# Kernel tuning notes

Measured on AMD Instinct MI355X. Metric: run time of the kernel, lower is better.

Reference implementation:

```python
import jax, jax.numpy as jnp
import numpy as np

B, T, C, H = 2, 2048, 1024, 16


def setup_inputs() -> dict:
    key = jax.random.key(0)
    ks = jax.random.split(key, 9)
    s = 1.0 / np.sqrt(C)
    return {
        "query": jax.random.normal(ks[0], (B, T, C), dtype=jnp.float32),
        "Wq": jax.random.normal(ks[1], (C, C), dtype=jnp.float32) * s,
        "bq": jnp.zeros((C,), dtype=jnp.float32),
        "Wk": jax.random.normal(ks[2], (C, C), dtype=jnp.float32) * s,
        "bk": jnp.zeros((C,), dtype=jnp.float32),
        "Wv": jax.random.normal(ks[3], (C, C), dtype=jnp.float32) * s,
        "bv": jnp.zeros((C,), dtype=jnp.float32),
        "Wp": jax.random.normal(ks[4], (C, C), dtype=jnp.float32) * s,
        "bp": jnp.zeros((C,), dtype=jnp.float32),
        "n_head": H,
    }


def reference(query, Wq, bq, Wk, bk, Wv, bv, Wp, bp, n_head):
    b, t, c = query.shape
    d = c // n_head
    # QKV projections -> [b, h, t, d]
    q = (query @ Wq + bq).reshape(b, t, n_head, d).transpose(0, 2, 1, 3)
    k = (query @ Wk + bk).reshape(b, t, n_head, d).transpose(0, 2, 1, 3)
    v = (query @ Wv + bv).reshape(b, t, n_head, d).transpose(0, 2, 1, 3)
    scale = 1.0 / jnp.sqrt(jnp.asarray(d, dtype=query.dtype))
    att = jnp.einsum('bhtd,bhsd->bhts', q, k) * scale  # [b,h,t,t]
    causal = jnp.tril(jnp.ones((t, t), dtype=bool))
    att = jnp.where(causal[None, None, :, :], att, -jnp.inf)
    att = jax.nn.softmax(att, axis=-1)
    y = jnp.einsum('bhts,bhsd->bhtd', att, v)  # [b,h,t,d]
    y = y.transpose(0, 2, 1, 3).reshape(b, t, c)
    return y @ Wp + bp
```

## Files before the change

### kernel.cpp

```cpp
#include <hip/hip_runtime.h>
#include <math.h>

#define B_ 2
#define T_ 2048
#define C_ 1024
#define H_ 16
#define D_ 64
#define M_ (B_*T_)

typedef __bf16 bf16x8 __attribute__((ext_vector_type(8)));
typedef __bf16 bf16x4 __attribute__((ext_vector_type(4)));
typedef float  f32x4  __attribute__((ext_vector_type(4)));

__device__ __forceinline__ unsigned short f2bf(float f) {
    unsigned int u = __float_as_uint(f);
    u += 0x7FFFu + ((u >> 16) & 1u);
    return (unsigned short)(u >> 16);
}

__device__ __forceinline__ void gload16(const void* g, void* l) {
    __builtin_amdgcn_global_load_lds(
        (const __attribute__((address_space(1))) void*)g,
        (__attribute__((address_space(3))) void*)l, 16, 0, 0);
}

__global__ __launch_bounds__(256) void prep_kernel(
    const float* __restrict__ X, unsigned short* __restrict__ Xb,
    const float* __restrict__ W0, const float* __restrict__ W1,
    const float* __restrict__ W2, const float* __restrict__ W3,
    unsigned short* __restrict__ T0, unsigned short* __restrict__ T1,
    unsigned short* __restrict__ T2, unsigned short* __restrict__ T3)
{
    const int tid = threadIdx.x;
    if (blockIdx.x < 2048) {
        const size_t i = ((size_t)blockIdx.x * 256 + tid) * 8;
        const float4 a = *(const float4*)&X[i];
        const float4 b = *(const float4*)&X[i + 4];
        ushort4 s0, s1;
        s0.x = f2bf(a.x); s0.y = f2bf(a.y); s0.z = f2bf(a.z); s0.w = f2bf(a.w);
        s1.x = f2bf(b.x); s1.y = f2bf(b.y); s1.z = f2bf(b.z); s1.w = f2bf(b.w);
        *(ushort4*)&Xb[i]     = s0;
        *(ushort4*)&Xb[i + 4] = s1;
        return;
    }
    const int bz = blockIdx.x - 2048;
    const int z = bz >> 10, rem = bz & 1023;
    const float* W; unsigned short* Wt;
    switch (z) {
        case 0: W = W0; Wt = T0; break;
        case 1: W = W1; Wt = T1; break;
        case 2: W = W2; Wt = T2; break;
        default: W = W3; Wt = T3; break;
    }
    __shared__ unsigned short tile[32][33];
    const int k0 = (rem >> 5) * 32, n0 = (rem & 31) * 32;
    {
        const int r = tid >> 3, c = (tid & 7) * 4;
        const float4 v = *(const float4*)&W[(size_t)(k0 + r)*C_ + n0 + c];
        tile[c+0][r] = f2bf(v.x);
        tile[c+1][r] = f2bf(v.y);
        tile[c+2][r] = f2bf(v.z);
        tile[c+3][r] = f2bf(v.w);
    }
    __syncthreads();
    {
        const int r = tid >> 3, c = (tid & 7) * 4;
        ushort4 s;
        s.x = tile[r][c+0]; s.y = tile[r][c+1]; s.z = tile[r][c+2]; s.w = tile[r][c+3];
        *(ushort4*)&Wt[(size_t)(n0 + r)*C_ + k0 + c] = s;
    }
}

__global__ __launch_bounds__(256) void gemm_mfma_kernel(
    const unsigned short* __restrict__ A, const unsigned short* __restrict__ Bt,
    const float* __restrict__ b0, const float* __restrict__ b1,
    const float* __restrict__ b2,
    void* __restrict__ out0, void* __restrict__ out1, void* __restrict__ out2,
    int mode)
{
    __shared__ __align__(16) unsigned short Als[2][128 * 32];
    __shared__ __align__(16) unsigned short Bls[2][128 * 32];

    const int tid  = threadIdx.x;
    const int lane = tid & 63;
    const int wave = tid >> 6;
    const int wm = wave >> 1, wn = wave & 1;
    const int l15 = lane & 15, quad = lane >> 4;
    const int m0 = blockIdx.y * 128, n0 = blockIdx.x * 128;
    const int srow = lane >> 2;
    const int scol = (lane & 3) * 8;

    const f32x4 zero4 = {0.f, 0.f, 0.f, 0.f};
    f32x4 acc[4][4];
    #pragma unroll
    for (int i = 0; i < 4; ++i)
        #pragma unroll
        for (int j = 0; j < 4; ++j) acc[i][j] = zero4;

    for (int k0 = 0; k0 < C_; k0 += 64) {
        __syncthreads();
        #pragma unroll
        for (int h = 0; h < 2; ++h) {
            #pragma unroll
            for (int u = 0; u < 2; ++u) {
                const int r = wave*32 + u*16 + srow;
                gload16(&A [(size_t)(m0 + r)*C_ + k0 + h*32 + scol],
                        &Als[h][(wave*32 + u*16)*32]);
                gload16(&Bt[(size_t)(n0 + r)*C_ + k0 + h*32 + scol],
                        &Bls[h][(wave*32 + u*16)*32]);
            }
        }
        __syncthreads();

        #pragma unroll
        for (int h = 0; h < 2; ++h) {
            bf16x8 af[4], bfr[4];
            #pragma unroll
            for (int i = 0; i < 4; ++i)
                af[i] = *(const bf16x8*)&Als[h][(wm*64 + i*16 + l15)*32 + quad*8];
            #pragma unroll
            for (int j = 0; j < 4; ++j)
                bfr[j] = *(const bf16x8*)&Bls[h][(wn*64 + j*16 + l15)*32 + quad*8];

            #pragma unroll
            for (int i = 0; i < 4; ++i)
                #pragma unroll
                for (int j = 0; j < 4; ++j)
                    acc[i][j] = __builtin_amdgcn_mfma_f32_16x16x32_bf16(
                        af[i], bfr[j], acc[i][j], 0, 0, 0);
        }
    }

    if (mode == 0) {
        float* o0 = (float*)out0;
        #pragma unroll
        for (int j = 0; j < 4; ++j) {
            const int n = n0 + wn*64 + j*16 + l15;
            const float bias = b0[n];
            #pragma unroll
            for (int i = 0; i < 4; ++i)
                #pragma unroll
                for (int r = 0; r < 4; ++r) {
                    const int m = m0 + wm*64 + i*16 + quad*4 + r;
                    o0[(size_t)m*C_ + n] = acc[i][j][r] + bias;
                }
        }
        return;
    }

    __syncthreads();
    unsigned short* Ep = (wave < 2) ? &Als[wave][0] : &Bls[wave - 2][0];

    const int which = n0 >> 10;
    const int c0 = n0 & (C_ - 1);
    const int h  = (c0 >> 6) + wn;
    const int bb = m0 >> 11;
    const int t0 = (m0 & (T_ - 1)) + wm*64;
    const int bh = bb*H_ + h;
    const float* bp = (which == 0) ? b0 : (which == 1 ? b1 : b2);
    const float qscale = (which == 0) ? 0.125f : 1.0f;

    if (which < 2) {
        #pragma unroll
        for (int j = 0; j < 4; ++j) {
            const int cl = j*16 + l15;
            const float bias = bp[c0 + wn*64 + cl];
            #pragma unroll
            for (int i = 0; i < 4; ++i)
                #pragma unroll
                for (int r = 0; r < 4; ++r)
                    Ep[(i*16 + quad*4 + r)*64 + cl] =
                        f2bf((acc[i][j][r] + bias) * qscale);
        }
        unsigned short* op = (which == 0) ? (unsigned short*)out0
                                          : (unsigned short*)out1;
        const int chunk = lane & 7;
        #pragma unroll
        for (int u = 0; u < 8; ++u) {
            const int row = u*8 + (lane >> 3);
            const uint4 v = *(const uint4*)&Ep[row*64 + chunk*8];
            *(uint4*)&op[((size_t)bh*T_ + t0 + row)*D_ + chunk*8] = v;
        }
    } else {
        #pragma unroll
        for (int j = 0; j < 4; ++j) {
            const int cl = j*16 + l15;
            const float bias = bp[c0 + wn*64 + cl];
            const int xo = (l15 & 7) * 8;
            #pragma unroll
            for (int i = 0; i < 4; ++i) {
                ushort4 pk;
                pk.x = f2bf(acc[i][j][0] + bias);
                pk.y = f2bf(acc[i][j][1] + bias);
                pk.z = f2bf(acc[i][j][2] + bias);
                pk.w = f2bf(acc[i][j][3] + bias);
                *(ushort4*)&Ep[cl*64 + ((i*16 + quad*4) ^ xo)] = pk;
            }
        }
        unsigned short* op = (unsigned short*)out2;
        const int chunk = lane & 7;
        #pragma unroll
        for (int u = 0; u < 8; ++u) {
            const int d = u*8 + (lane >> 3);
            const uint4 v = *(const uint4*)&Ep[d*64 + ((chunk*8) ^ ((d & 7)*8))];
            *(uint4*)&op[((size_t)bh*D_ + d)*T_ + t0 + chunk*8] = v;
        }
    }
}

__global__ __launch_bounds__(256) void flash_mfma_kernel(
    const unsigned short* __restrict__ Qs, const unsigned short* __restrict__ Ks,
    const unsigned short* __restrict__ Vts, unsigned short* __restrict__ Y,
    float* __restrict__ parts, float* __restrict__ lbase)
{
    __shared__ __align__(16) unsigned short Kls[64 * 64];
    __shared__ __align__(16) unsigned short Vls[64 * 64];
    __shared__ __align__(16) unsigned short Pls[4 * 2048];

    const int tid  = threadIdx.x;
    const int lane = tid & 63, wave = tid >> 6;
    const int l15  = lane & 15, quad = lane >> 4;
    const int job  = blockIdx.x >> 5;
    const int bh   = blockIdx.x & 31;
    const bool isA = (job < 8);
    const int a    = isA ? job : job - 8;

    int qts[2], slos[2], shis[2], slots[2], nseg;
    if (isA) {
        qts[0] = a;      slos[0] = 0;        shis[0] = 2*a + 2;  slots[0] = -1;
        qts[1] = 15 - a; slos[1] = 0;        shis[1] = 15 - 2*a; slots[1] = 0;
        nseg = 2;
    } else {
        qts[0] = 15 - a; slos[0] = 15 - 2*a; shis[0] = 32 - 2*a; slots[0] = 1;
        nseg = 1;
    }

    unsigned short* Pw = &Pls[wave * 2048];
    const int kd_s = wave >> 1;
    const int c8_s = (kd_s * 4 + quad) * 8;
    const int b_ = bh >> 4, h_ = bh & (H_ - 1);
    const f32x4 zero4 = {0.f, 0.f, 0.f, 0.f};

    for (int sg = 0; sg < nseg; ++sg) {
        const int qt  = qts[sg];
        const int qw0 = qt * 128 + wave * 32;

        bf16x8 qf[2][2];
        #pragma unroll
        for (int i = 0; i < 2; ++i)
            #pragma unroll
            for (int kd = 0; kd < 2; ++kd)
                qf[i][kd] = *(const bf16x8*)&Qs[((size_t)bh*T_ + qw0 + i*16 + l15)*D_
                                                + kd*32 + quad*8];

        f32x4 o[2][4];
        #pragma unroll
        for (int i = 0; i < 2; ++i)
            #pragma unroll
            for (int jd = 0; jd < 4; ++jd) o[i][jd] = zero4;
        float lsum[2] = {0.f, 0.f};

        for (int it = slos[sg]; it < shis[sg]; ++it) {
            const int s0 = it * 64;
            __syncthreads();
            #pragma unroll
            for (int u = 0; u < 2; ++u) {
                const int cu  = 2*wave + u;
                const int row = ((cu & 3) << 4) + l15;
                gload16(&Ks [((size_t)bh*T_ + s0 + row)*D_ + c8_s],
                        (char*)Kls + cu*1024);
                gload16(&Vts[((size_t)bh*D_ + row)*T_ + s0 + c8_s],
                        (char*)Vls + cu*1024);
            }
            __syncthreads();

            if (s0 > qw0 + 31) continue;

            f32x4 st[2][4];
            #pragma unroll
            for (int i = 0; i < 2; ++i)
                #pragma unroll
                for (int j = 0; j < 4; ++j) st[i][j] = zero4;
            #pragma unroll
            for (int kd = 0; kd < 2; ++kd) {
                bf16x8 kf[4];
                #pragma unroll
                for (int j = 0; j < 4; ++j)
                    kf[j] = *(const bf16x8*)&Kls[lane*8 + j*512 + kd*2048];
                #pragma unroll
                for (int i = 0; i < 2; ++i)
                    #pragma unroll
                    for (int j = 0; j < 4; ++j)
                        st[i][j] = __builtin_amdgcn_mfma_f32_16x16x32_bf16(
                            kf[j], qf[i][kd], st[i][j], 0, 0, 0);
            }

            const bool diag = (s0 + 63 > qw0);
            #pragma unroll
            for (int i = 0; i < 2; ++i) {
                const int qrow = qw0 + i*16 + l15;
                #pragma unroll
                for (int j = 0; j < 4; ++j)
                    #pragma unroll
                    for (int r = 0; r < 4; ++r) {
                        float e = __expf(st[i][j][r]);
                        if (diag && (s0 + j*16 + quad*4 + r > qrow)) e = 0.f;
                        st[i][j][r] = e;
                        lsum[i] += e;
                    }
            }

            #pragma unroll
            for (int i = 0; i < 2; ++i)
                #pragma unroll
                for (int j = 0; j < 4; ++j) {
                    bf16x4 pk = {(__bf16)st[i][j][0], (__bf16)st[i][j][1],
                                 (__bf16)st[i][j][2], (__bf16)st[i][j][3]};
                    *(bf16x4*)&Pw[(((j>>1)*2 + i)*4 + (j&1)*2 + (quad>>1))*128
                                   + l15*8 + (quad&1)*4] = pk;
                }

            #pragma unroll
            for (int kk = 0; kk < 2; ++kk) {
                bf16x8 pf[2], vf[4];
                #pragma unroll
                for (int i = 0; i < 2; ++i)
                    pf[i] = *(const bf16x8*)&Pw[(kk*2 + i)*512 + lane*8];
                #pragma unroll
                for (int jd = 0; jd < 4; ++jd)
                    vf[jd] = *(const bf16x8*)&Vls[lane*8 + jd*512 + kk*2048];
                #pragma unroll
                for (int i = 0; i < 2; ++i)
                    #pragma unroll
                    for (int jd = 0; jd < 4; ++jd)
                        o[i][jd] = __builtin_amdgcn_mfma_f32_16x16x32_bf16(
                            vf[jd], pf[i], o[i][jd], 0, 0, 0);
            }
        }

        #pragma unroll
        for (int i = 0; i < 2; ++i) {
            float v = lsum[i];
            v += __shfl_xor(v, 16, 64);
            v += __shfl_xor(v, 32, 64);
            lsum[i] = v;
        }

        if (slots[sg] < 0) {
            #pragma unroll
            for (int i = 0; i < 2; ++i) {
                const float inv = 1.0f / lsum[i];
                const int t = qw0 + i*16 + l15;
                #pragma unroll
                for (int jd = 0; jd < 4; ++jd) {
                    bf16x4 pk = {(__bf16)(o[i][jd][0] * inv),
                                 (__bf16)(o[i][jd][1] * inv),
                                 (__bf16)(o[i][jd][2] * inv),
                                 (__bf16)(o[i][jd][3] * inv)};
                    *(bf16x4*)&Y[((size_t)(b_*T_ + t))*C_ + h_*D_ + jd*16 + quad*4]
                        = pk;
                }
            }
        } else {
            const int gpi = bh*16 + a*2 + slots[sg];
            float* Op = parts + (size_t)gpi*8192;
            float* Lp = lbase + gpi*128;
            #pragma unroll
            for (int i = 0; i < 2; ++i) {
                const int tl = wave*32 + i*16 + l15;
                if (quad == 0) Lp[tl] = lsum[i];
                #pragma unroll
                for (int jd = 0; jd < 4; ++jd)
                    *(f32x4*)&Op[(size_t)tl*64 + jd*16 + quad*4] = o[i][jd];
            }
        }
    }
}

__global__ __launch_bounds__(256) void merge_kernel(
    const float* __restrict__ parts, const float* __restrict__ lbase,
    unsigned short* __restrict__ Y)
{
    const int pair = blockIdx.x;
    const int bh = pair >> 3, p = pair & 7;
    const int qt = 15 - p;
    const int g0 = bh*16 + p*2;
    const float* O0 = parts + (size_t)g0*8192;
    const float* O1 = O0 + 8192;
    const float* L0 = lbase + g0*128;
    const float* L1 = L0 + 128;

    const int tid = threadIdx.x;
    const int r = tid >> 1, c0 = (tid & 1) * 32;
    const float inv = 1.0f / (L0[r] + L1[r]);
    const int b = bh >> 4, h = bh & (H_ - 1);
    const int t = qt*128 + r;
    #pragma unroll
    for (int k = 0; k < 8; ++k) {
        const f32x4 a  = *(const f32x4*)&O0[(size_t)r*64 + c0 + k*4];
        const f32x4 bb = *(const f32x4*)&O1[(size_t)r*64 + c0 + k*4];
        bf16x4 pk = {(__bf16)((a[0]+bb[0])*inv), (__bf16)((a[1]+bb[1])*inv),
                     (__bf16)((a[2]+bb[2])*inv), (__bf16)((a[3]+bb[3])*inv)};
        *(bf16x4*)&Y[((size_t)(b*T_ + t))*C_ + h*D_ + c0 + k*4] = pk;
    }
}

extern "C" void kernel_launch(void* const* d_in, const int* in_sizes, int n_in,
                              void* d_out, int out_size, void* d_ws, size_t ws_size,
                              hipStream_t stream) {
    const float* query = (const float*)d_in[0];
    const float* Wq = (const float*)d_in[1];
    const float* bq = (const float*)d_in[2];
    const float* Wk = (const float*)d_in[3];
    const float* bk = (const float*)d_in[4];
    const float* Wv = (const float*)d_in[5];
    const float* bv = (const float*)d_in[6];
    const float* Wp = (const float*)d_in[7];
    const float* bp = (const float*)d_in[8];
    float* out = (float*)d_out;

    char* ws = (char*)d_ws;
    unsigned short* qbf   = (unsigned short*)(ws);
    unsigned short* kbf   = (unsigned short*)(ws + 8388608);
    unsigned short* vtbf  = (unsigned short*)(ws + 16777216);
    unsigned short* WtP   = (unsigned short*)(ws + 25165824);
    unsigned short* WtQKV = (unsigned short*)(ws + 27262976);
    unsigned short* yb    = (unsigned short*)(ws + 33554432);
    unsigned short* qx    = (unsigned short*)(ws + 41943040);
    float* lbase = (float*)(ws + 27262976);
    float* parts = out;

    prep_kernel<<<6144, 256, 0, stream>>>(
        query, qx, Wq, Wk, Wv, Wp,
        WtQKV, WtQKV + (size_t)C_*C_, WtQKV + 2*(size_t)C_*C_, WtP);

    gemm_mfma_kernel<<<dim3(3*C_/128, M_/128), 256, 0, stream>>>(
        qx, WtQKV, bq, bk, bv, qbf, kbf, vtbf, 1);

    flash_mfma_kernel<<<512, 256, 0, stream>>>(qbf, kbf, vtbf, yb, parts, lbase);
    merge_kernel<<<256, 256, 0, stream>>>(parts, lbase, yb);

    gemm_mfma_kernel<<<dim3(C_/128, M_/128), 256, 0, stream>>>(
        yb, WtP, bp, bp, bp, out, nullptr, nullptr, 0);
}
```

Measured before the change: 209.4 us.

## Fuse split-KV merge into flash kernel via atomic counters; process two KV tiles per barrier

Removes the separate merge kernel launch: each flash block that writes a partial result bumps a per-(bh, query-tile) atomic counter, and the second finisher merges both partials into Y. Counters are zeroed by an extra block in the prep kernel. The flash inner loop also loads two K/V tiles per sync pair into doubled LDS buffers, halving barrier count but increasing LDS use, which may reduce occupancy.

```diff
diff --git a/kernel.cpp b/kernel.cpp
--- a/kernel.cpp
+++ b/kernel.cpp
@@ -29,9 +29,14 @@
     const float* __restrict__ W0, const float* __restrict__ W1,
     const float* __restrict__ W2, const float* __restrict__ W3,
     unsigned short* __restrict__ T0, unsigned short* __restrict__ T1,
-    unsigned short* __restrict__ T2, unsigned short* __restrict__ T3)
+    unsigned short* __restrict__ T2, unsigned short* __restrict__ T3,
+    int* __restrict__ counters)
 {
     const int tid = threadIdx.x;
+    if (blockIdx.x == 6144) {
+        if (tid < 256) counters[tid] = 0;
+        return;
+    }
     if (blockIdx.x < 2048) {
         const size_t i = ((size_t)blockIdx.x * 256 + tid) * 8;
         const float4 a = *(const float4*)&X[i];
@@ -211,11 +216,13 @@
 __global__ __launch_bounds__(256) void flash_mfma_kernel(
     const unsigned short* __restrict__ Qs, const unsigned short* __restrict__ Ks,
     const unsigned short* __restrict__ Vts, unsigned short* __restrict__ Y,
-    float* __restrict__ parts, float* __restrict__ lbase)
+    float* __restrict__ parts, float* __restrict__ lbase,
+    int* __restrict__ counters)
 {
-    __shared__ __align__(16) unsigned short Kls[64 * 64];
-    __shared__ __align__(16) unsigned short Vls[64 * 64];
+    __shared__ __align__(16) unsigned short Kls[2][64 * 64];
+    __shared__ __align__(16) unsigned short Vls[2][64 * 64];
     __shared__ __align__(16) unsigned short Pls[4 * 2048];
+    __shared__ int doMerge;
 
     const int tid  = threadIdx.x;
     const int lane = tid & 63, wave = tid >> 6;
@@ -240,6 +247,7 @@
     const int c8_s = (kd_s * 4 + quad) * 8;
     const int b_ = bh >> 4, h_ = bh & (H_ - 1);
     const f32x4 zero4 = {0.f, 0.f, 0.f, 0.f};
+    bool wrotePartial = false;
 
     for (int sg = 0; sg < nseg; ++sg) {
         const int qt  = qts[sg];
@@ -260,81 +268,97 @@
             for (int jd = 0; jd < 4; ++jd) o[i][jd] = zero4;
         float lsum[2] = {0.f, 0.f};
 
-        for (int it = slos[sg]; it < shis[sg]; ++it) {
-            const int s0 = it * 64;
+        for (int it = slos[sg]; it < shis[sg]; it += 2) {
+            const bool two = (it + 1 < shis[sg]);
             __syncthreads();
             #pragma unroll
             for (int u = 0; u < 2; ++u) {
                 const int cu  = 2*wave + u;
                 const int row = ((cu & 3) << 4) + l15;
-                gload16(&Ks [((size_t)bh*T_ + s0 + row)*D_ + c8_s],
-                        (char*)Kls + cu*1024);
-                gload16(&Vts[((size_t)bh*D_ + row)*T_ + s0 + c8_s],
-                        (char*)Vls + cu*1024);
+                gload16(&Ks [((size_t)bh*T_ + it*64 + row)*D_ + c8_s],
+                        (char*)&Kls[0][0] + cu*1024);
+                gload16(&Vts[((size_t)bh*D_ + row)*T_ + it*64 + c8_s],
+                        (char*)&Vls[0][0] + cu*1024);
+            }
+            if (two) {
+                #pragma unroll
+                for (int u = 0; u < 2; ++u) {
+                    const int cu  = 2*wave + u;
+                    const int row = ((cu & 3) << 4) + l15;
+                    gload16(&Ks [((size_t)bh*T_ + (it+1)*64 + row)*D_ + c8_s],
+                            (char*)&Kls[1][0] + cu*1024);
+                    gload16(&Vts[((size_t)bh*D_ + row)*T_ + (it+1)*64 + c8_s],
+                            (char*)&Vls[1][0] + cu*1024);
+                }
             }
             __syncthreads();
 
-            if (s0 > qw0 + 31) continue;
-
-            f32x4 st[2][4];
-            #pragma unroll
-            for (int i = 0; i < 2; ++i)
-                #pragma unroll
-                for (int j = 0; j < 4; ++j) st[i][j] = zero4;
-            #pragma unroll
-            for (int kd = 0; kd < 2; ++kd) {
-                bf16x8 kf[4];
-                #pragma unroll
-                for (int j = 0; j < 4; ++j)
-                    kf[j] = *(const bf16x8*)&Kls[lane*8 + j*512 + kd*2048];
+            #pragma unroll
+            for (int tt = 0; tt < 2; ++tt) {
+                if (tt && !two) break;
+                const int s0 = (it + tt) * 64;
+                if (s0 > qw0 + 31) continue;
+
+                f32x4 st[2][4];
                 #pragma unroll
                 for (int i = 0; i < 2; ++i)
                     #pragma unroll
+                    for (int j = 0; j < 4; ++j) st[i][j] = zero4;
+                #pragma unroll
+                for (int kd = 0; kd < 2; ++kd) {
+                    bf16x8 kf[4];
+                    #pragma unroll
                     for (int j = 0; j < 4; ++j)
-                        st[i][j] = __builtin_amdgcn_mfma_f32_16x16x32_bf16(
-                            kf[j], qf[i][kd], st[i][j], 0, 0, 0);
-            }
-
-            const bool diag = (s0 + 63 > qw0);
-            #pragma unroll
-            for (int i = 0; i < 2; ++i) {
-                const int qrow = qw0 + i*16 + l15;
-                #pragma unroll
-                for (int j = 0; j < 4; ++j)
-                    #pragma unroll
-                    for (int r = 0; r < 4; ++r) {
-                        float e = __expf(st[i][j][r]);
-                        if (diag && (s0 + j*16 + quad*4 + r > qrow)) e = 0.f;
-                        st[i][j][r] = e;
-                        lsum[i] += e;
+                        kf[j] = *(const bf16x8*)&Kls[tt][lane*8 + j*512 + kd*2048];
+                    #pragma unroll
+                    for (int i = 0; i < 2; ++i)
+                        #pragma unroll
+                        for (int j = 0; j < 4; ++j)
+                            st[i][j] = __builtin_amdgcn_mfma_f32_16x16x32_bf16(
+                                kf[j], qf[i][kd], st[i][j], 0, 0, 0);
+                }
+
+                const bool diag = (s0 + 63 > qw0);
+                #pragma unroll
+                for (int i = 0; i < 2; ++i) {
+                    const int qrow = qw0 + i*16 + l15;
+                    #pragma unroll
+                    for (int j = 0; j < 4; ++j)
+                        #pragma unroll
+                        for (int r = 0; r < 4; ++r) {
+                            float e = __expf(st[i][j][r]);
+                            if (diag && (s0 + j*16 + quad*4 + r > qrow)) e = 0.f;
+                            st[i][j][r] = e;
+                            lsum[i] += e;
+                        }
+                }
+
+                #pragma unroll
+                for (int i = 0; i < 2; ++i)
+                    #pragma unroll
+                    for (int j = 0; j < 4; ++j) {
+                        bf16x4 pk = {(__bf16)st[i][j][0], (__bf16)st[i][j][1],
+                                     (__bf16)st[i][j][2], (__bf16)st[i][j][3]};
+                        *(bf16x4*)&Pw[(((j>>1)*2 + i)*4 + (j&1)*2 + (quad>>1))*128
+                                       + l15*8 + (quad&1)*4] = pk;
                     }
-            }
-
-            #pragma unroll
-            for (int i = 0; i < 2; ++i)
-                #pragma unroll
-                for (int j = 0; j < 4; ++j) {
-                    bf16x4 pk = {(__bf16)st[i][j][0], (__bf16)st[i][j][1],
-                                 (__bf16)st[i][j][2], (__bf16)st[i][j][3]};
-                    *(bf16x4*)&Pw[(((j>>1)*2 + i)*4 + (j&1)*2 + (quad>>1))*128
-                                   + l15*8 + (quad&1)*4] = pk;
-                }
-
-            #pragma unroll
-            for (int kk = 0; kk < 2; ++kk) {
-                bf16x8 pf[2], vf[4];
-                #pragma unroll
-                for (int i = 0; i < 2; ++i)
-                    pf[i] = *(const bf16x8*)&Pw[(kk*2 + i)*512 + lane*8];
-                #pragma unroll
-                for (int jd = 0; jd < 4; ++jd)
-                    vf[jd] = *(const bf16x8*)&Vls[lane*8 + jd*512 + kk*2048];
-                #pragma unroll
-                for (int i = 0; i < 2; ++i)
+
+                #pragma unroll
+                for (int kk = 0; kk < 2; ++kk) {
+                    bf16x8 pf[2], vf[4];
+                    #pragma unroll
+                    for (int i = 0; i < 2; ++i)
+                        pf[i] = *(const bf16x8*)&Pw[(kk*2 + i)*512 + lane*8];
                     #pragma unroll
                     for (int jd = 0; jd < 4; ++jd)
-                        o[i][jd] = __builtin_amdgcn_mfma_f32_16x16x32_bf16(
-                            vf[jd], pf[i], o[i][jd], 0, 0, 0);
+                        vf[jd] = *(const bf16x8*)&Vls[tt][lane*8 + jd*512 + kk*2048];
+                    #pragma unroll
+                    for (int i = 0; i < 2; ++i)
+                        #pragma unroll
+                        for (int jd = 0; jd < 4; ++jd)
+                            o[i][jd] = __builtin_amdgcn_mfma_f32_16x16x32_bf16(
+                                vf[jd], pf[i], o[i][jd], 0, 0, 0);
+                }
             }
         }
 
@@ -350,7 +374,7 @@
             #pragma unroll
             for (int i = 0; i < 2; ++i) {
                 const float inv = 1.0f / lsum[i];
-                const int t = qw0 + i*16 + l15;
+                const int t = qts[sg]*128 + wave*32 + i*16 + l15;
                 #pragma unroll
                 for (int jd = 0; jd < 4; ++jd) {
                     bf16x4 pk = {(__bf16)(o[i][jd][0] * inv),
@@ -373,35 +397,40 @@
                 for (int jd = 0; jd < 4; ++jd)
                     *(f32x4*)&Op[(size_t)tl*64 + jd*16 + quad*4] = o[i][jd];
             }
-        }
-    }
-}
-
-__global__ __launch_bounds__(256) void merge_kernel(
-    const float* __restrict__ parts, const float* __restrict__ lbase,
-    unsigned short* __restrict__ Y)
-{
-    const int pair = blockIdx.x;
-    const int bh = pair >> 3, p = pair & 7;
-    const int qt = 15 - p;
-    const int g0 = bh*16 + p*2;
-    const float* O0 = parts + (size_t)g0*8192;
-    const float* O1 = O0 + 8192;
-    const float* L0 = lbase + g0*128;
-    const float* L1 = L0 + 128;
-
-    const int tid = threadIdx.x;
-    const int r = tid >> 1, c0 = (tid & 1) * 32;
-    const float inv = 1.0f / (L0[r] + L1[r]);
-    const int b = bh >> 4, h = bh & (H_ - 1);
-    const int t = qt*128 + r;
-    #pragma unroll
-    for (int k = 0; k < 8; ++k) {
-        const f32x4 a  = *(const f32x4*)&O0[(size_t)r*64 + c0 + k*4];
-        const f32x4 bb = *(const f32x4*)&O1[(size_t)r*64 + c0 + k*4];
-        bf16x4 pk = {(__bf16)((a[0]+bb[0])*inv), (__bf16)((a[1]+bb[1])*inv),
-                     (__bf16)((a[2]+bb[2])*inv), (__bf16)((a[3]+bb[3])*inv)};
-        *(bf16x4*)&Y[((size_t)(b*T_ + t))*C_ + h*D_ + c0 + k*4] = pk;
+            wrotePartial = true;
+        }
+    }
+
+    if (wrotePartial) {
+        __syncthreads();
+        if (tid == 0) {
+            __threadfence();
+            const int old = atomicAdd(&counters[bh*8 + a], 1);
+            doMerge = (old == 1);
+        }
+        __syncthreads();
+        if (doMerge) {
+            __threadfence();
+            const int qt = 15 - a;
+            const int g0 = bh*16 + a*2;
+            const float* O0 = parts + (size_t)g0*8192;
+            const float* O1 = O0 + 8192;
+            const float* L0 = lbase + g0*128;
+            const float* L1 = L0 + 128;
+            const int r = tid >> 1, c0m = (tid & 1) * 32;
+            const float inv = 1.0f / (L0[r] + L1[r]);
+            const int t = qt*128 + r;
+            #pragma unroll
+            for (int k = 0; k < 8; ++k) {
+                const f32x4 x0 = *(const f32x4*)&O0[(size_t)r*64 + c0m + k*4];
+                const f32x4 x1 = *(const f32x4*)&O1[(size_t)r*64 + c0m + k*4];
+                bf16x4 pk = {(__bf16)((x0[0]+x1[0])*inv),
+                             (__bf16)((x0[1]+x1[1])*inv),
+                             (__bf16)((x0[2]+x1[2])*inv),
+                             (__bf16)((x0[3]+x1[3])*inv)};
+                *(bf16x4*)&Y[((size_t)(b_*T_ + t))*C_ + h_*D_ + c0m + k*4] = pk;
+            }
+        }
     }
 }
 
@@ -427,18 +456,19 @@
     unsigned short* WtQKV = (unsigned short*)(ws + 27262976);
     unsigned short* yb    = (unsigned short*)(ws + 33554432);
     unsigned short* qx    = (unsigned short*)(ws + 41943040);
-    float* lbase = (float*)(ws + 27262976);
-    float* parts = out;
-
-    prep_kernel<<<6144, 256, 0, stream>>>(
+    float* lbase    = (float*)(ws + 27262976);
+    int*   counters = (int*)  (ws + 50331648);
+    float* parts    = out;
+
+    prep_kernel<<<6145, 256, 0, stream>>>(
         query, qx, Wq, Wk, Wv, Wp,
-        WtQKV, WtQKV + (size_t)C_*C_, WtQKV + 2*(size_t)C_*C_, WtP);
+        WtQKV, WtQKV + (size_t)C_*C_, WtQKV + 2*(size_t)C_*C_, WtP, counters);
 
     gemm_mfma_kernel<<<dim3(3*C_/128, M_/128), 256, 0, stream>>>(
         qx, WtQKV, bq, bk, bv, qbf, kbf, vtbf, 1);
 
-    flash_mfma_kernel<<<512, 256, 0, stream>>>(qbf, kbf, vtbf, yb, parts, lbase);
-    merge_kernel<<<256, 256, 0, stream>>>(parts, lbase, yb);
+    flash_mfma_kernel<<<512, 256, 0, stream>>>(qbf, kbf, vtbf, yb,
+                                               parts, lbase, counters);
 
     gemm_mfma_kernel<<<dim3(C_/128, M_/128), 256, 0, stream>>>(
         yb, WtP, bp, bp, bp, out, nullptr, nullptr, 0);
```

After: 246.1 us. +17.5%, slower.
